# Optimization experiments

Hardware: AMD Instinct MI355X
Metric: run time of the kernel (lower is better)

## Reference

```python
import jax, jax.numpy as jnp
import numpy as np

TEMPERATURE = 0.1
NORM_EPS = 1e-12          # F.normalize default eps
SMALL_VAL = float(np.finfo(np.float32).tiny)  # pytorch-metric-learning small_val(float32)
NEG_INF = float(np.finfo(np.float32).min)     # c_f.neg_inf for masked logsumexp


def setup_inputs() -> dict:
    key = jax.random.key(0)
    k1, k2 = jax.random.split(key)
    N, D = 8192, 128
    emb = jax.random.normal(k1, (N, D), dtype=jnp.float32)
    labels = jax.random.randint(k2, (N,), 0, 1000, dtype=jnp.int64)
    return {"emb": emb, "labels": labels}


def reference(emb, labels):
    N = emb.shape[0]
    # F.normalize(emb, dim=1): x / max(||x||, eps)
    norms = jnp.linalg.norm(emb, axis=1, keepdims=True)
    x = emb / jnp.maximum(norms, NORM_EPS)

    # cosine similarity matrix [N, N], scaled by temperature
    mat = jnp.matmul(x, x.T) / TEMPERATURE

    same = labels[:, None] == labels[None, :]
    diag = jnp.eye(N, dtype=bool)
    pos_mask = same & ~diag          # same label, i != j
    keep_mask = ~diag                # pos + neg (all off-diagonal)

    # numerical stability: subtract detached row max (over full row, incl. diagonal)
    mat_max = jax.lax.stop_gradient(jnp.max(mat, axis=1, keepdims=True))
    mat = mat - mat_max

    # masked logsumexp over off-diagonal entries
    masked = jnp.where(keep_mask, mat, NEG_INF)
    denom = jax.nn.logsumexp(masked, axis=1, keepdims=True)  # [N, 1]

    log_prob = mat - denom
    pos_f = pos_mask.astype(mat.dtype)
    mean_log_prob_pos = jnp.sum(pos_f * log_prob, axis=1) / (
        jnp.sum(pos_f, axis=1) + SMALL_VAL
    )
    losses = -mean_log_prob_pos  # per-element losses
    # SumReducer: sum over elements
    return jnp.sum(losses)
```

## Files before the change

### kernel.cpp

```cpp
#include <hip/hip_runtime.h>
#include <hip/hip_bf16.h>


typedef __bf16 bf16_t;
typedef __bf16 bf16x2 __attribute__((ext_vector_type(2)));
typedef __bf16 bf16x8 __attribute__((ext_vector_type(8)));
typedef float f32x16 __attribute__((ext_vector_type(16)));

#define NN 8192
#define DIM 128
#define SWEEP 16
#define SMALL_VAL 1.17549435e-38f
#define L2E10 14.4269504089f
#define LN2 0.69314718056f

__device__ inline size_t swz(int row, int lane) {
    int f = lane >> 3, hh = (lane >> 2) & 1, j = (lane & 3) << 1;
    return ((size_t)(row >> 5) * 4096) + f * 512 + hh * 256 + (row & 31) * 8 + j;
}

#define DPPADD(v, ctrl, rmask)                                                         \
    do {                                                                               \
        int _t = __builtin_amdgcn_update_dpp(0, __float_as_int((v)), (ctrl), (rmask),  \
                                             0xf, true);                               \
        (v) += __int_as_float(_t);                                                     \
    } while (0)

__device__ inline float half32_sum(float v) {
    DPPADD(v, 0x111, 0xf);
    DPPADD(v, 0x112, 0xf);
    DPPADD(v, 0x114, 0xf);
    DPPADD(v, 0x118, 0xf);
    DPPADD(v, 0x142, 0xa);
    return v;
}

__device__ inline void gload_lds16(const bf16_t* g, bf16_t* l) {
    __builtin_amdgcn_global_load_lds(
        (const __attribute__((address_space(1))) unsigned int*)g,
        (__attribute__((address_space(3))) unsigned int*)l, 16, 0, 0);
}

__global__ __launch_bounds__(256) void norm_csum(const float* __restrict__ emb,
                                                 const int* __restrict__ labels,
                                                 bf16_t* __restrict__ xsw,
                                                 float* __restrict__ cd_arr,
                                                 float* __restrict__ sd_arr,
                                                 float* __restrict__ cm1_arr,
                                                 float* __restrict__ out) {
    __shared__ float cs[DIM];
    __shared__ int rowlist[96];
    __shared__ int nrows;
    int cls = blockIdx.x;
    int wv = threadIdx.x >> 6, lane = threadIdx.x & 63;
    if (threadIdx.x < DIM) cs[threadIdx.x] = 0.f;
    if (threadIdx.x == 0) nrows = 0;
    if (cls == 0 && threadIdx.x == 0) *out = 0.f;
    __syncthreads();

    float s0 = 0.f, s1 = 0.f;
    const int4* lab4 = (const int4*)(labels + wv * 2048);
#pragma unroll
    for (int it = 0; it < 8; ++it) {
        int4 l = lab4[it * 64 + lane];
        int base = wv * 2048 + it * 256;
#pragma unroll
        for (int cmp = 0; cmp < 4; ++cmp) {
            int li = (cmp == 0) ? l.x : (cmp == 1) ? l.y : (cmp == 2) ? l.z : l.w;
            unsigned long long m = __ballot(li == cls);
            while (m) {
                int bb = __builtin_ctzll(m);
                m &= m - 1;
                int row = base + 4 * bb + cmp;
                float2 v = ((const float2*)emb)[row * 64 + lane];
                float ss = fmaf(v.x, v.x, v.y * v.y);
#pragma unroll
                for (int mm = 1; mm < 64; mm <<= 1) ss += __shfl_xor(ss, mm, 64);
                float inv = 1.0f / fmaxf(sqrtf(ss), 1e-12f);
                bf16x2 o; o.x = (bf16_t)(v.x * inv); o.y = (bf16_t)(v.y * inv);
                *(bf16x2*)(xsw + swz(row, lane)) = o;
                s0 += (float)o.x; s1 += (float)o.y;
                if (lane == 0) {
                    int idx = atomicAdd(&nrows, 1);
                    if (idx < 96) rowlist[idx] = row;
                }
            }
        }
    }
    atomicAdd(&cs[2 * lane], s0);
    atomicAdd(&cs[2 * lane + 1], s1);
    __syncthreads();
    int n = nrows;
    for (int k = wv; k < n; k += 4) {
        int row = rowlist[k];
        bf16x2 xv = *(const bf16x2*)(xsw + swz(row, lane));
        float x0 = (float)xv.x, x1 = (float)xv.y;
        float cdp = fmaf(x0, cs[2 * lane], x1 * cs[2 * lane + 1]);
        float sdp = fmaf(x0, x0, x1 * x1);
#pragma unroll
        for (int mm = 1; mm < 64; mm <<= 1) {
            cdp += __shfl_xor(cdp, mm, 64);
            sdp += __shfl_xor(sdp, mm, 64);
        }
        if (lane == 0) {
            cd_arr[row] = cdp; sd_arr[row] = sdp; cm1_arr[row] = (float)(n - 1);
        }
    }
}

__global__
__attribute__((amdgpu_flat_work_group_size(256, 256)))
__attribute__((amdgpu_waves_per_eu(4, 4)))
void supcon_sweep(const bf16_t* __restrict__ xsw,
                  float* __restrict__ se_part) {
    __shared__ bf16_t bst[4 * 4096];

    int s = blockIdx.x & 15, bg = blockIdx.x >> 4;
    int wv = threadIdx.x >> 6, lane = threadIdx.x & 63;
    int I = bg * 4 + wv;
    int c = lane & 31, h = lane >> 5;
    int laneoff = h * 256 + c * 8;

    const bf16_t* abase = xsw + (size_t)I * 4096 + laneoff;
    bf16x8 a[8];
#pragma unroll
    for (int f = 0; f < 8; ++f) a[f] = *(const bf16x8*)(abase + f * 512);

    float se[16];
#pragma unroll
    for (int r = 0; r < 16; ++r) se[r] = 0.f;

#pragma unroll 1
    for (int k = 0; k < 4; ++k) {
        {
            const bf16_t* gsrc = xsw + (size_t)(s + 16 * k) * 16384;
#pragma unroll
            for (int i = 0; i < 8; ++i) {
                int kk = i * 4 + wv;
                gload_lds16(gsrc + kk * 512 + lane * 8, bst + kk * 512);
            }
        }
        __syncthreads();

#pragma unroll
        for (int t = 0; t < 4; ++t) {
            f32x16 acc;
#pragma unroll
            for (int r = 0; r < 16; ++r) acc[r] = 0.f;
            const bf16_t* bt = bst + t * 4096 + laneoff;
#pragma unroll
            for (int f = 0; f < 8; ++f) {
                bf16x8 bfr = *(const bf16x8*)(bt + f * 512);
                acc = __builtin_amdgcn_mfma_f32_32x32x16_bf16(a[f], bfr, acc, 0, 0, 0);
            }
#pragma unroll
            for (int r = 0; r < 16; ++r)
                se[r] += __builtin_amdgcn_exp2f(fmaf(acc[r], L2E10, -L2E10));
        }
        __syncthreads();
    }

#pragma unroll
    for (int r = 0; r < 16; ++r) se[r] = half32_sum(se[r]);
    if (c == 31) {
        float* dst = se_part + (size_t)s * NN + I * 32 + 4 * h;
#pragma unroll
        for (int r = 0; r < 16; ++r)
            dst[(r & 3) + 8 * (r >> 2)] = se[r];
    }
}

__global__ __launch_bounds__(256) void finalize_kernel(const float* __restrict__ se_part,
                                                       const float* __restrict__ cd_arr,
                                                       const float* __restrict__ sd_arr,
                                                       const float* __restrict__ cm1_arr,
                                                       float* __restrict__ out) {
    __shared__ float part[4];
    int i = blockIdx.x * 256 + threadIdx.x;
    float sev_raw = 0.f;
#pragma unroll
    for (int s = 0; s < SWEEP; ++s) sev_raw += se_part[(size_t)s * NN + i];
    float sd = sd_arr[i], cd = cd_arr[i], cm1 = cm1_arr[i];
    float diag = __builtin_amdgcn_exp2f(fmaf(sd, L2E10, -L2E10));
    float sev  = fmaxf(sev_raw - diag, 1e-30f);
    float lse  = fmaf(__builtin_amdgcn_logf(sev), LN2, 10.f);
    float loss = (cm1 * lse - 10.f * (cd - sd)) / (cm1 + SMALL_VAL);
#pragma unroll
    for (int m = 1; m < 64; m <<= 1) loss += __shfl_xor(loss, m, 64);
    int wv = threadIdx.x >> 6;
    if ((threadIdx.x & 63) == 0) part[wv] = loss;
    __syncthreads();
    if (threadIdx.x == 0) atomicAdd(out, part[0] + part[1] + part[2] + part[3]);
}

extern "C" void kernel_launch(void* const* d_in, const int* in_sizes, int n_in,
                              void* d_out, int out_size, void* d_ws, size_t ws_size,
                              hipStream_t stream) {
    const float* emb  = (const float*)d_in[0];
    const int* labels = (const int*)d_in[1];

    char* ws = (char*)d_ws;
    bf16_t* xsw   = (bf16_t*)ws;
    float* separt = (float*)(ws + (size_t)NN * DIM * 2);
    float* cd     = separt + (size_t)SWEEP * NN;
    float* sd     = cd + NN;
    float* cm1    = sd + NN;

    norm_csum<<<1024, 256, 0, stream>>>(emb, labels, xsw, cd, sd, cm1, (float*)d_out);
    supcon_sweep<<<1024, 256, 0, stream>>>(xsw, separt);
    finalize_kernel<<<NN / 256, 256, 0, stream>>>(separt, cd, sd, cm1, (float*)d_out);
}
```

Before: 94.25 us.

## Double-buffer LDS tiles and widen sweep blocks to eight waves

Supcon sweep blocks now hold eight waves, so each staged B-tile is reused by twice as many row tiles. The B tiles are double-buffered in LDS, with the next tile's load issued before computing on the current one. The MFMA chain is split into two independent accumulators to shorten dependency stalls. The costs are higher LDS use per block and reliance on the barrier to wait for the async loads.

```diff
diff --git a/kernel.cpp b/kernel.cpp
--- a/kernel.cpp
+++ b/kernel.cpp
@@ -109,15 +109,15 @@
 }
 
 __global__
-__attribute__((amdgpu_flat_work_group_size(256, 256)))
+__attribute__((amdgpu_flat_work_group_size(512, 512)))
 __attribute__((amdgpu_waves_per_eu(4, 4)))
 void supcon_sweep(const bf16_t* __restrict__ xsw,
                   float* __restrict__ se_part) {
-    __shared__ bf16_t bst[4 * 4096];
-
-    int s = blockIdx.x & 15, bg = blockIdx.x >> 4;
+    __shared__ bf16_t bst[2][4 * 4096];
+
+    int s = blockIdx.x & 15, rb = blockIdx.x >> 4;
     int wv = threadIdx.x >> 6, lane = threadIdx.x & 63;
-    int I = bg * 4 + wv;
+    int I = rb * 8 + wv;
     int c = lane & 31, h = lane >> 5;
     int laneoff = h * 256 + c * 8;
 
@@ -130,32 +130,45 @@
 #pragma unroll
     for (int r = 0; r < 16; ++r) se[r] = 0.f;
 
+    {
+        const bf16_t* gsrc = xsw + (size_t)s * 16384;
+#pragma unroll
+        for (int i = 0; i < 4; ++i) {
+            int kk = i * 8 + wv;
+            gload_lds16(gsrc + kk * 512 + lane * 8, &bst[0][kk * 512]);
+        }
+    }
+    __syncthreads();
+
 #pragma unroll 1
     for (int k = 0; k < 4; ++k) {
-        {
-            const bf16_t* gsrc = xsw + (size_t)(s + 16 * k) * 16384;
-#pragma unroll
-            for (int i = 0; i < 8; ++i) {
-                int kk = i * 4 + wv;
-                gload_lds16(gsrc + kk * 512 + lane * 8, bst + kk * 512);
+        if (k < 3) {
+            const bf16_t* gsrc = xsw + (size_t)(s + 16 * (k + 1)) * 16384;
+            bf16_t* dbuf = &bst[(k + 1) & 1][0];
+#pragma unroll
+            for (int i = 0; i < 4; ++i) {
+                int kk = i * 8 + wv;
+                gload_lds16(gsrc + kk * 512 + lane * 8, dbuf + kk * 512);
             }
         }
-        __syncthreads();
+        const bf16_t* bb = &bst[k & 1][0];
 
 #pragma unroll
         for (int t = 0; t < 4; ++t) {
-            f32x16 acc;
-#pragma unroll
-            for (int r = 0; r < 16; ++r) acc[r] = 0.f;
-            const bf16_t* bt = bst + t * 4096 + laneoff;
-#pragma unroll
-            for (int f = 0; f < 8; ++f) {
-                bf16x8 bfr = *(const bf16x8*)(bt + f * 512);
-                acc = __builtin_amdgcn_mfma_f32_32x32x16_bf16(a[f], bfr, acc, 0, 0, 0);
+            f32x16 acc0, acc1;
+#pragma unroll
+            for (int r = 0; r < 16; ++r) { acc0[r] = 0.f; acc1[r] = 0.f; }
+            const bf16_t* bt = bb + t * 4096 + laneoff;
+#pragma unroll
+            for (int f = 0; f < 8; f += 2) {
+                bf16x8 b0 = *(const bf16x8*)(bt + f * 512);
+                bf16x8 b1 = *(const bf16x8*)(bt + (f + 1) * 512);
+                acc0 = __builtin_amdgcn_mfma_f32_32x32x16_bf16(a[f], b0, acc0, 0, 0, 0);
+                acc1 = __builtin_amdgcn_mfma_f32_32x32x16_bf16(a[f + 1], b1, acc1, 0, 0, 0);
             }
 #pragma unroll
             for (int r = 0; r < 16; ++r)
-                se[r] += __builtin_amdgcn_exp2f(fmaf(acc[r], L2E10, -L2E10));
+                se[r] += __builtin_amdgcn_exp2f(fmaf(acc0[r] + acc1[r], L2E10, -L2E10));
         }
         __syncthreads();
     }
@@ -207,6 +220,6 @@
     float* cm1    = sd + NN;
 
     norm_csum<<<1024, 256, 0, stream>>>(emb, labels, xsw, cd, sd, cm1, (float*)d_out);
-    supcon_sweep<<<1024, 256, 0, stream>>>(xsw, separt);
+    supcon_sweep<<<512, 512, 0, stream>>>(xsw, separt);
     finalize_kernel<<<NN / 256, 256, 0, stream>>>(separt, cd, sd, cm1, (float*)d_out);
 }
```

Measured after the change: 118.8 us. 26.0% more time.
